# Optimization experiments

Measured on AMD Instinct MI355X. Metric: run time of the kernel, lower is better.

Reference implementation:

```python
import jax, jax.numpy as jnp
import numpy as np

N = 50000; E = 800000; T = 800000; G = 64
H = 128; IEMB = 128; BAS = 8; NS = 4; NR = 6; OEH = 128; OUT = 1; NB = 4; CUT = 5.0


def envelope(x):
    # exponent=5 -> p=6: 1/x + a*x^5 + b*x^6 + c*x^7 with a=-28, b=48, c=-21
    return 1.0 / x - 28.0 * x**5 + 48.0 * x**6 - 21.0 * x**7


def setup_inputs() -> dict:
    key = jax.random.key(0)
    ks = iter(jax.random.split(key, 80))
    def w(shape, s=0.1):
        return jax.random.normal(next(ks), shape, dtype=jnp.float32) * s
    inp = {}
    inp['z'] = jax.random.randint(next(ks), (N,), 0, 100, dtype=jnp.int32)
    inp['dist'] = jax.random.uniform(next(ks), (E,), jnp.float32, 0.05, 1.0)
    inp['dist_trip'] = jax.random.uniform(next(ks), (T,), jnp.float32, 0.05, 1.0)
    inp['angle'] = jax.random.uniform(next(ks), (T,), jnp.float32, -1.0, 1.0)
    inp['edge_index'] = jax.random.randint(next(ks), (2, E), 0, N, dtype=jnp.int32)
    inp['triplets'] = jax.random.randint(next(ks), (T, 3), 0, N, dtype=jnp.int32)
    inp['batch'] = jnp.sort(jax.random.randint(next(ks), (N,), 0, G, dtype=jnp.int32))
    inp['atom_table'] = w((100, H), 1.0)
    inp['rbf_freq'] = jnp.arange(1, NR + 1, dtype=jnp.float32) * jnp.float32(np.pi)
    inp['sbf_freq'] = jnp.arange(1, NR + 1, dtype=jnp.float32) * jnp.float32(np.pi)
    inp['emb_w1'] = w((NR, IEMB)); inp['emb_b1'] = w((IEMB,), 0.01)
    inp['emb_w2'] = w((IEMB, H)); inp['emb_b2'] = w((H,), 0.01)
    inp['iw_rbf1'] = w((NB, NR, BAS)); inp['iw_rbf2'] = w((NB, BAS, H))
    inp['iw_sbf1'] = w((NB, NS * NR, BAS)); inp['iw_sbf2'] = w((NB, BAS, IEMB))
    inp['iw_t1'] = w((NB, H, IEMB)); inp['iw_t2'] = w((NB, IEMB, H)); inp['ib_t2'] = w((NB, H), 0.01)
    inp['iw_up'] = w((NB, H, H)); inp['ib_up'] = w((NB, H), 0.01)
    inp['iw_down'] = w((NB, H, H)); inp['ib_down'] = w((NB, H), 0.01)
    inp['ow_rbf'] = w((NB + 1, NR, H))
    inp['ow0'] = w((NB + 1, H, OEH)); inp['ob0'] = w((NB + 1, OEH), 0.01)
    inp['ow1'] = w((NB + 1, OEH, OEH)); inp['ob1'] = w((NB + 1, OEH), 0.01)
    inp['ow2'] = w((NB + 1, OEH, OUT)); inp['ob2'] = w((NB + 1, OUT), 0.01)
    return inp


def _forward(atom_table, rbf_freq, sbf_freq, emb_w1, emb_b1, emb_w2, emb_b2,
             iw_rbf1, iw_rbf2, iw_sbf1, iw_sbf2, iw_t1, iw_t2, ib_t2,
             iw_up, ib_up, iw_down, ib_down, ow_rbf, ow0, ob0, ow1, ob1, ow2, ob2,
             dist, dist_trip, angle, z, edge_index, triplets, batch):
    row, col = edge_index[0], edge_index[1]
    j_idx = triplets[:, 1]
    # radial basis for edges: [E, NR]
    d = dist[:, None] / CUT
    rbf_e = envelope(d) * jnp.sin(rbf_freq * d)
    # spherical basis for triplets: [T, NS*NR]
    dt = dist_trip[:, None] / CUT
    rbf_t = envelope(dt) * jnp.sin(sbf_freq * dt)
    a = angle[:, None]
    sph = jnp.concatenate([jnp.ones_like(a), a, 0.5 * (3 * a**2 - 1), 0.5 * (5 * a**3 - 3 * a)], axis=-1)
    sbf_t = (rbf_t[:, None, :] * sph[:, :, None]).reshape(a.shape[0], -1)

    x = atom_table[z]  # [N, H]
    # EmbeddingBlock: edge msg from rbf only, scattered to col
    e = jax.nn.silu(rbf_e @ emb_w1 + emb_b1) @ emb_w2 + emb_b2
    x = x + jax.ops.segment_sum(e, col, num_segments=N)

    def out_block(k, x):
        rbf_emb = rbf_e @ ow_rbf[k]            # [E, H]
        h = jax.ops.segment_sum(x[row] * rbf_emb, col, num_segments=N)
        h = jax.nn.silu(h @ ow0[k] + ob0[k])
        h = jax.nn.silu(h @ ow1[k] + ob1[k])
        return h @ ow2[k] + ob2[k]             # [N, OUT]

    P = out_block(0, x)
    for b in range(NB):
        x_up = x @ iw_up[b] + ib_up[b]
        x_down = x @ iw_down[b] + ib_down[b]
        rbf_emb = jax.nn.silu(rbf_e @ iw_rbf1[b]) @ iw_rbf2[b]      # [E, H]
        x_edge = x_up[row] * rbf_emb                                  # [E, H]
        sbf_emb = jax.nn.silu(sbf_t @ iw_sbf1[b]) @ iw_sbf2[b]      # [T, H]
        t = jax.nn.silu(x_down @ iw_t1[b]) @ iw_t2[b] + ib_t2[b]     # [N, H]
        # original: for each triplet i, x_edge += t[j]*sbf_emb[i] (broadcast over all edges)
        extra = jnp.sum(t[j_idx] * sbf_emb, axis=0)                   # [H]
        x_edge = x_edge + extra
        x = x + jax.ops.segment_sum(x_edge, col, num_segments=N)
        P = P + out_block(b + 1, x)

    counts = jax.ops.segment_sum(jnp.ones((x.shape[0],), jnp.float32), batch, num_segments=G)
    pooled = jax.ops.segment_sum(P, batch, num_segments=G) / jnp.maximum(counts, 1.0)[:, None]
    return pooled  # [G, OUT]


def reference(z, dist, dist_trip, angle, edge_index, triplets, batch, atom_table, rbf_freq, sbf_freq,
              emb_w1, emb_b1, emb_w2, emb_b2, iw_rbf1, iw_rbf2, iw_sbf1, iw_sbf2, iw_t1, iw_t2, ib_t2,
              iw_up, ib_up, iw_down, ib_down, ow_rbf, ow0, ob0, ow1, ob1, ow2, ob2):
    return _forward(atom_table, rbf_freq, sbf_freq, emb_w1, emb_b1, emb_w2, emb_b2,
                    iw_rbf1, iw_rbf2, iw_sbf1, iw_sbf2, iw_t1, iw_t2, ib_t2,
                    iw_up, ib_up, iw_down, ib_down, ow_rbf, ow0, ob0, ow1, ob1, ow2, ob2,
                    dist, dist_trip, angle, z, edge_index, triplets, batch)
```

## Files before the change

kernel.cpp:

```cpp
#include <hip/hip_runtime.h>
#include <hip/hip_fp16.h>

#define N_ 50000
#define E_ 800000
#define T_ 800000
#define G_ 64
#define H_ 128

#define NBK 782
#define NSB (NBK * 8)
#define CAPS 512
#define CHUNK 4096
#define EB ((E_ + CHUNK - 1) / CHUNK)
#define TB ((T_ + CHUNK - 1) / CHUNK)
#define XSLOT 16

#define GEMMG2 ((N_ + 31) / 32)
#define NG2 ((N_ + 1) / 2)
#define NIX ((N_ * 16 + 127) / 128)
#define SVG ((N_ + 3) / 4)
#define EG ((E_ + 255) / 256)
#define TG ((T_ + 255) / 256)

typedef __attribute__((ext_vector_type(8))) short bf16x8;
typedef __attribute__((ext_vector_type(4))) float f32x4;
typedef _Float16 f16x2 __attribute__((ext_vector_type(2)));

__device__ __forceinline__ float siluf(float v) {
    return __fdividef(v, 1.0f + __expf(-v));
}

__device__ __forceinline__ unsigned short f2bf(float f) {
    unsigned int u = __float_as_uint(f);
    u += 0x7fffu + ((u >> 16) & 1u);
    return (unsigned short)(u >> 16);
}
__device__ __forceinline__ unsigned int f2bf2(float a, float b) {
    return (unsigned int)f2bf(a) | ((unsigned int)f2bf(b) << 16);
}
__device__ __forceinline__ float bf2f(unsigned short h) {
    return __uint_as_float(((unsigned int)h) << 16);
}
__device__ __forceinline__ float2 bf2x2(unsigned int p) {
    return make_float2(__uint_as_float(p << 16), __uint_as_float(p & 0xffff0000u));
}
__device__ __forceinline__ float fdot2f(f16x2 a, f16x2 b, float c) {
    return __builtin_amdgcn_fdot2(a, b, c, false);
}

__global__ __launch_bounds__(256) void k_bucket(const int* __restrict__ ecol,
                                                const int* __restrict__ trip,
                                                int* bcntE, unsigned int* __restrict__ ebkt,
                                                int* bcntT, unsigned int* __restrict__ tbkt) {
    __shared__ int hist[NBK];
    __shared__ int bbase[NBK];
    int blk = blockIdx.x;
    bool isE = blk < EB;
    int ebase = (isE ? blk : blk - EB) * CHUNK;
    const int nElem = isE ? E_ : T_;
    int r = blk & 7;
    int* bcnt = isE ? bcntE : bcntT;
    unsigned int* bkt = isE ? ebkt : tbkt;
    int tid = threadIdx.x;

    for (int i = tid; i < NBK; i += 256) hist[i] = 0;
    __syncthreads();

    int cols[16];
    #pragma unroll
    for (int u = 0; u < 16; ++u) {
        int idx = ebase + u * 256 + tid;
        int c = -1;
        if (idx < nElem) c = isE ? ecol[idx] : trip[3 * idx + 1];
        cols[u] = c;
        if (c >= 0) atomicAdd(&hist[c >> 6], 1);
    }
    __syncthreads();

    for (int b = tid; b < NBK; b += 256) {
        int c = hist[b];
        bbase[b] = c ? atomicAdd(&bcnt[b * 8 + r], c) : 0;
        hist[b] = 0;
    }
    __syncthreads();

    #pragma unroll
    for (int u = 0; u < 16; ++u) {
        int c = cols[u];
        if (c >= 0) {
            int bk = c >> 6;
            int off = atomicAdd(&hist[bk], 1);
            int pos = bbase[bk] + off;
            if (pos < CAPS) {
                int idx = ebase + u * 256 + tid;
                bkt[(size_t)(bk * 8 + r) * CAPS + pos] =
                    ((unsigned int)idx << 6) | (unsigned int)(c & 63);
            }
        }
    }
}

__global__ __launch_bounds__(1024) void k_scanB(const int* __restrict__ bcntE, int* bktbaseE,
                                                const int* __restrict__ bcntT, int* bktbaseT) {
    const int* bcnt = (blockIdx.x == 0) ? bcntE : bcntT;
    int* bb = (blockIdx.x == 0) ? bktbaseE : bktbaseT;
    int tid = threadIdx.x, lane = tid & 63, w = tid >> 6;
    __shared__ int wsum[16];
    int v = 0;
    if (tid < NBK) {
        #pragma unroll
        for (int s = 0; s < 8; ++s) v += min(bcnt[tid * 8 + s], CAPS);
    }
    int incl = v;
    #pragma unroll
    for (int s = 1; s < 64; s <<= 1) {
        int t = __shfl_up(incl, (unsigned)s, 64);
        if (lane >= s) incl += t;
    }
    if (lane == 63) wsum[w] = incl;
    __syncthreads();
    int wexcl = 0;
    for (int j = 0; j < w; ++j) wexcl += wsum[j];
    if (tid < NBK) bb[tid] = wexcl + incl - v;
}

__global__ __launch_bounds__(256) void k_place(const int* __restrict__ bcntE, const unsigned int* __restrict__ ebkt,
                                               const int* __restrict__ erow, const float* __restrict__ dist,
                                               const int* __restrict__ bktbaseE, int* __restrict__ rowptrE,
                                               int* __restrict__ slist, float* __restrict__ distS,
                                               const int* __restrict__ bcntT, const unsigned int* __restrict__ tbkt,
                                               const float* __restrict__ dist_trip, const float* __restrict__ angle,
                                               const int* __restrict__ bktbaseT, int* __restrict__ rowptrT,
                                               float2* __restrict__ tpay) {
    int b = blockIdx.x;
    bool isE = b < NBK;
    if (!isE) b -= NBK;
    int tid = threadIdx.x;
    __shared__ int ccnt[64];
    __shared__ int cbase[64];
    __shared__ int nb[8];
    if (tid < 64) ccnt[tid] = 0;
    const int* bcnt = isE ? bcntE : bcntT;
    const unsigned int* bkt = isE ? ebkt : tbkt;
    if (tid < 8) nb[tid] = min(bcnt[b * 8 + tid], CAPS);
    __syncthreads();
    for (int s = 0; s < 8; ++s) {
        int n = nb[s];
        const unsigned int* src = bkt + (size_t)(b * 8 + s) * CAPS;
        for (int i = tid; i < n; i += 256) atomicAdd(&ccnt[src[i] & 63u], 1);
    }
    __syncthreads();
    if (tid < 64) {
        int v = ccnt[tid];
        int incl = v;
        #pragma unroll
        for (int s = 1; s < 64; s <<= 1) {
            int t = __shfl_up(incl, (unsigned)s, 64);
            if (tid >= s) incl += t;
        }
        int base = (isE ? bktbaseE : bktbaseT)[b];
        int excl = base + incl - v;
        cbase[tid] = excl;
        int col = b * 64 + tid;
        int* rp = isE ? rowptrE : rowptrT;
        if (col <= N_) rp[col] = excl;
        ccnt[tid] = 0;
    }
    __syncthreads();
    for (int s = 0; s < 8; ++s) {
        int n = nb[s];
        const unsigned int* src = bkt + (size_t)(b * 8 + s) * CAPS;
        for (int i = tid; i < n; i += 256) {
            unsigned int rec = src[i];
            int c = (int)(rec & 63u);
            int e = (int)(rec >> 6);
            int off = atomicAdd(&ccnt[c], 1);
            int pos = cbase[c] + off;
            if (isE) {
                slist[pos] = erow[e];
                distS[pos] = dist[e];
            } else {
                tpay[pos] = make_float2(dist_trip[e], angle[e]);
            }
        }
    }
}

__global__ __launch_bounds__(256) void k_wprep(const float* __restrict__ emb_w2, const float* __restrict__ iw_down,
                                               const float* __restrict__ iw_t1, const float* __restrict__ iw_t2,
                                               const float* __restrict__ iw_up, const float* __restrict__ ow0,
                                               const float* __restrict__ ow1, unsigned short* __restrict__ Wt) {
    int mat = blockIdx.x >> 3;
    int part = blockIdx.x & 7;
    const float* src;
    if (mat == 0) src = emb_w2;
    else if (mat < 5) src = iw_down + (size_t)(mat - 1) * 16384;
    else if (mat < 9) src = iw_t1 + (size_t)(mat - 5) * 16384;
    else if (mat < 13) src = iw_t2 + (size_t)(mat - 9) * 16384;
    else if (mat < 17) src = iw_up + (size_t)(mat - 13) * 16384;
    else if (mat < 22) src = ow0 + (size_t)(mat - 17) * 16384;
    else src = ow1 + (size_t)(mat - 22) * 16384;
    unsigned short* dst = Wt + (size_t)mat * 16384;
    int base = part * 2048;
    for (int i = base + threadIdx.x; i < base + 2048; i += 256) {
        int k = i >> 7, n = i & 127;
        dst[n * 128 + k] = f2bf(src[i]);
    }
}

__global__ __launch_bounds__(256) void k_geomb(const float* __restrict__ distS,
                                               const float* __restrict__ freq, const float* __restrict__ iw_rbf1,
                                               float* __restrict__ rbfS, __half* __restrict__ s8all,
                                               const float2* __restrict__ tpay, const float* __restrict__ sfreq,
                                               __half* __restrict__ basis) {
    __shared__ float W1s[4][48];
    int tid = threadIdx.x;
    if (blockIdx.x < EG) {
        if (tid < 192) W1s[tid / 48][tid % 48] = iw_rbf1[tid];
        __syncthreads();
        int p = blockIdx.x * 256 + tid;
        if (p >= E_) return;
        float d = distS[p] * 0.2f;
        float d2 = d * d, d4 = d2 * d2, d5 = d4 * d;
        float env = __fdividef(1.0f, d) - 28.0f * d5 + 48.0f * d5 * d - 21.0f * d5 * d2;
        float rb[6];
        #pragma unroll
        for (int r = 0; r < 6; ++r) {
            rb[r] = env * __sinf(freq[r] * d);
            rbfS[(size_t)p * 6 + r] = rb[r];
        }
        #pragma unroll
        for (int b = 0; b < 4; ++b) {
            __half out[8];
            #pragma unroll
            for (int k = 0; k < 8; ++k) {
                float u = 0.f;
                #pragma unroll
                for (int r = 0; r < 6; ++r) u += rb[r] * W1s[b][r * 8 + k];
                out[k] = __float2half(siluf(u));
            }
            *(uint4*)&s8all[((size_t)b * E_ + p) * 8] = *(uint4*)out;
        }
    } else {
        int t = (blockIdx.x - EG) * 256 + tid;
        if (t >= T_) return;
        float2 da = tpay[t];
        float d = da.x * 0.2f;
        float a = da.y;
        float d2 = d * d, d4 = d2 * d2, d5 = d4 * d;
        float env = __fdividef(1.0f, d) - 28.0f * d5 + 48.0f * d5 * d - 21.0f * d5 * d2;
        float rb[6];
        #pragma unroll
        for (int r = 0; r < 6; ++r) rb[r] = env * __sinf(sfreq[r] * d);
        float sph[4];
        sph[0] = 1.0f; sph[1] = a; sph[2] = 1.5f * a * a - 0.5f; sph[3] = 2.5f * a * a * a - 1.5f * a;
        __half out[24];
        #pragma unroll
        for (int s = 0; s < 4; ++s)
            #pragma unroll
            for (int r = 0; r < 6; ++r) out[s * 6 + r] = __float2half(sph[s] * rb[r]);
        uint4* dst = (uint4*)(basis + (size_t)t * 24);
        dst[0] = ((uint4*)out)[0];
        dst[1] = ((uint4*)out)[1];
        dst[2] = ((uint4*)out)[2];
    }
}

__global__ __launch_bounds__(128) void k_embSix(const float* __restrict__ atab, const int* __restrict__ z,
                                                unsigned short* __restrict__ xh,
                                                const int* __restrict__ rowptr, const float* __restrict__ rbfS,
                                                const float* __restrict__ w1, const float* __restrict__ b1,
                                                unsigned short* __restrict__ SSh) {
    int tid = threadIdx.x;
    if (blockIdx.x < NIX) {
        int t = blockIdx.x * 128 + tid;
        if (t >= N_ * 16) return;
        int node = t >> 4, q = t & 15;
        const float4* a4 = (const float4*)atab;
        float4 v0 = a4[(size_t)z[node] * 32 + q * 2];
        float4 v1 = a4[(size_t)z[node] * 32 + q * 2 + 1];
        uint4 pk;
        pk.x = f2bf2(v0.x, v0.y);
        pk.y = f2bf2(v0.z, v0.w);
        pk.z = f2bf2(v1.x, v1.y);
        pk.w = f2bf2(v1.z, v1.w);
        ((uint4*)xh)[t] = pk;
    } else {
        int node = (blockIdx.x - NIX) * 2 + (tid >> 6);
        int lane = tid & 63;
        if (node >= N_) return;
        int c = lane * 2;
        float wc0[6], wc1[6];
        #pragma unroll
        for (int r = 0; r < 6; ++r) { wc0[r] = w1[r * 128 + c]; wc1[r] = w1[r * 128 + c + 1]; }
        float bb0 = b1[c], bb1 = b1[c + 1];
        float a0 = 0.f, a1 = 0.f;
        int p0 = rowptr[node], p1 = rowptr[node + 1];
        int p = p0;
        for (; p + 4 <= p1; p += 4) {
            float2 rb[4][3];
            #pragma unroll
            for (int u = 0; u < 4; ++u) {
                const float2* r2 = (const float2*)&rbfS[(size_t)(p + u) * 6];
                rb[u][0] = r2[0]; rb[u][1] = r2[1]; rb[u][2] = r2[2];
            }
            #pragma unroll
            for (int u = 0; u < 4; ++u) {
                float u0 = bb0 + rb[u][0].x * wc0[0] + rb[u][0].y * wc0[1] + rb[u][1].x * wc0[2] +
                           rb[u][1].y * wc0[3] + rb[u][2].x * wc0[4] + rb[u][2].y * wc0[5];
                float u1 = bb1 + rb[u][0].x * wc1[0] + rb[u][0].y * wc1[1] + rb[u][1].x * wc1[2] +
                           rb[u][1].y * wc1[3] + rb[u][2].x * wc1[4] + rb[u][2].y * wc1[5];
                a0 += siluf(u0);
                a1 += siluf(u1);
            }
        }
        for (; p < p1; ++p) {
            const float2* r2 = (const float2*)&rbfS[(size_t)p * 6];
            float2 ra = r2[0], rbx = r2[1], rc = r2[2];
            float u0 = bb0 + ra.x * wc0[0] + ra.y * wc0[1] + rbx.x * wc0[2] + rbx.y * wc0[3] + rc.x * wc0[4] + rc.y * wc0[5];
            float u1 = bb1 + ra.x * wc1[0] + ra.y * wc1[1] + rbx.x * wc1[2] + rbx.y * wc1[3] + rc.x * wc1[4] + rc.y * wc1[5];
            a0 += siluf(u0);
            a1 += siluf(u1);
        }
        *(unsigned int*)&SSh[(size_t)node * 128 + c] = f2bf2(a0, a1);
    }
}


__device__ __forceinline__ void body_gemm(int bid, const unsigned short* Ap, const unsigned short* Wt,
                                          const float* bias, const int* rp, unsigned short* Ch, int M) {
    int tid = threadIdx.x;
    int wave = tid >> 6, lane = tid & 63;
    int m15 = lane & 15, quad = lane >> 4;
    int row0 = bid * 32 + wave * 16;
    int arow = row0 + m15;
    if (arow > M - 1) arow = M - 1;

    f32x4 acc[8];
    #pragma unroll
    for (int nt = 0; nt < 8; ++nt) acc[nt] = (f32x4){0.f, 0.f, 0.f, 0.f};
    #pragma unroll
    for (int kt = 0; kt < 4; ++kt) {
        int ks = kt * 32 + quad * 8;
        bf16x8 av = *(const bf16x8*)(Ap + (size_t)arow * 128 + ks);
        #pragma unroll
        for (int nt = 0; nt < 8; ++nt) {
            bf16x8 bf = *(const bf16x8*)(Wt + (size_t)(nt * 16 + m15) * 128 + ks);
            acc[nt] = __builtin_amdgcn_mfma_f32_16x16x32_bf16(av, bf, acc[nt], 0, 0, 0);
        }
    }
    #pragma unroll
    for (int nt = 0; nt < 8; ++nt) {
        int col = nt * 16 + m15;
        float bc = bias[col];
        #pragma unroll
        for (int reg = 0; reg < 4; ++reg) {
            int row = row0 + quad * 4 + reg;
            if (row < M) {
                float v = acc[nt][reg] + bc * (float)(rp[row + 1] - rp[row]);
                v += bf2f(Ch[(size_t)row * 128 + col]);
                Ch[(size_t)row * 128 + col] = f2bf(v);
            }
        }
    }
}

__device__ __forceinline__ void body_sv4(int bid, const int* rowptrT, const __half* basis,
                                         const float* iw_sbf1, float* SV4, int n) {
    int tid = threadIdx.x;
    int wave = tid >> 6, lane = tid & 63;
    int node = bid * 4 + wave * 2 + (lane >> 5);
    int sub = lane & 31;
    int blk = sub >> 3, k = sub & 7;
    if (node >= n) return;
    const float* W1 = iw_sbf1 + blk * 192;
    f16x2 w[12];
    #pragma unroll
    for (int j = 0; j < 12; ++j) {
        f16x2 t;
        t.x = (_Float16)W1[(2 * j) * 8 + k];
        t.y = (_Float16)W1[(2 * j + 1) * 8 + k];
        w[j] = t;
    }
    float acc = 0.f;
    int p0 = rowptrT[node], p1 = rowptrT[node + 1];
    for (int p = p0; p < p1; ++p) {
        union { uint4 q[3]; f16x2 h[12]; } bs;
        const uint4* bp = (const uint4*)(basis + (size_t)p * 24);
        bs.q[0] = bp[0]; bs.q[1] = bp[1]; bs.q[2] = bp[2];
        float u = 0.f;
        #pragma unroll
        for (int j = 0; j < 12; ++j) u = fdot2f(bs.h[j], w[j], u);
        acc += siluf(u);
    }
    SV4[((size_t)blk * n + node) * 8 + k] = acc;
}

__device__ __forceinline__ void body_gather(int node0, const int* rowptr, const int* slist,
                                            const float* rbfS, const unsigned short* xh,
                                            const float* wrbf, unsigned short* hB, int n) {
    int tid = threadIdx.x;
    int node = node0 + (tid >> 6);
    int lane = tid & 63;
    if (node >= n) return;
    int c = lane * 2;
    float wc0[6], wc1[6];
    #pragma unroll
    for (int r = 0; r < 6; ++r) { wc0[r] = wrbf[r * 128 + c]; wc1[r] = wrbf[r * 128 + c + 1]; }
    float a0 = 0.f, a1 = 0.f;
    int p0 = rowptr[node], p1 = rowptr[node + 1];
    int p = p0;
    for (; p + 4 <= p1; p += 4) {
        int s0 = slist[p], s1 = slist[p + 1], s2 = slist[p + 2], s3 = slist[p + 3];
        float2 rb[4][3];
        #pragma unroll
        for (int u = 0; u < 4; ++u) {
            const float2* r2 = (const float2*)&rbfS[(size_t)(p + u) * 6];
            rb[u][0] = r2[0]; rb[u][1] = r2[1]; rb[u][2] = r2[2];
        }
        unsigned int xv0 = *(const unsigned int*)&xh[(size_t)s0 * 128 + c];
        unsigned int xv1 = *(const unsigned int*)&xh[(size_t)s1 * 128 + c];
        unsigned int xv2 = *(const unsigned int*)&xh[(size_t)s2 * 128 + c];
        unsigned int xv3 = *(const unsigned int*)&xh[(size_t)s3 * 128 + c];
        #pragma unroll
        for (int u = 0; u < 4; ++u) {
            float e0 = rb[u][0].x * wc0[0] + rb[u][0].y * wc0[1] + rb[u][1].x * wc0[2] +
                       rb[u][1].y * wc0[3] + rb[u][2].x * wc0[4] + rb[u][2].y * wc0[5];
            float e1 = rb[u][0].x * wc1[0] + rb[u][0].y * wc1[1] + rb[u][1].x * wc1[2] +
                       rb[u][1].y * wc1[3] + rb[u][2].x * wc1[4] + rb[u][2].y * wc1[5];
            float2 xf = bf2x2((u == 0) ? xv0 : (u == 1) ? xv1 : (u == 2) ? xv2 : xv3);
            a0 += xf.x * e0;
            a1 += xf.y * e1;
        }
    }
    for (; p < p1; ++p) {
        int src = slist[p];
        const float2* r2 = (const float2*)&rbfS[(size_t)p * 6];
        float2 ra = r2[0], rbx = r2[1], rc = r2[2];
        float e0 = ra.x * wc0[0] + ra.y * wc0[1] + rbx.x * wc0[2] + rbx.y * wc0[3] + rc.x * wc0[4] + rc.y * wc0[5];
        float e1 = ra.x * wc1[0] + ra.y * wc1[1] + rbx.x * wc1[2] + rbx.y * wc1[3] + rc.x * wc1[4] + rc.y * wc1[5];
        float2 xf = bf2x2(*(const unsigned int*)&xh[(size_t)src * 128 + c]);
        a0 += xf.x * e0;
        a1 += xf.y * e1;
    }
    *(unsigned int*)&hB[(size_t)node * 128 + c] = f2bf2(a0, a1);
}

__device__ __forceinline__ void body_block_mlp(int bid, unsigned short* smh,
                                               const unsigned short* xh,
                                               const unsigned short* Wd, const float* bd,
                                               const unsigned short* Wt1,
                                               const unsigned short* Wt2, const float* bt2,
                                               const unsigned short* Wup, const float* bup,
                                               const float* SV, const float* W2,
                                               float* extraP, unsigned short* xuph, int M) {
    int tid = threadIdx.x;
    int wave = tid >> 6, lane = tid & 63;
    int m15 = lane & 15, quad = lane >> 4;
    int row0 = bid * 32 + wave * 16;
    int arow = row0 + m15;
    if (arow > M - 1) arow = M - 1;
    unsigned short* L = smh + wave * (16 * 136);

    f32x4 accD[8], accU[8];
    #pragma unroll
    for (int nt = 0; nt < 8; ++nt) { accD[nt] = (f32x4){0.f, 0.f, 0.f, 0.f}; accU[nt] = (f32x4){0.f, 0.f, 0.f, 0.f}; }
    #pragma unroll
    for (int kt = 0; kt < 4; ++kt) {
        int ks = kt * 32 + quad * 8;
        bf16x8 av = *(const bf16x8*)(xh + (size_t)arow * 128 + ks);
        #pragma unroll
        for (int nt = 0; nt < 8; ++nt) {
            bf16x8 bd_ = *(const bf16x8*)(Wd + (size_t)(nt * 16 + m15) * 128 + ks);
            accD[nt] = __builtin_amdgcn_mfma_f32_16x16x32_bf16(av, bd_, accD[nt], 0, 0, 0);
            bf16x8 bu_ = *(const bf16x8*)(Wup + (size_t)(nt * 16 + m15) * 128 + ks);
            accU[nt] = __builtin_amdgcn_mfma_f32_16x16x32_bf16(av, bu_, accU[nt], 0, 0, 0);
        }
    }
    #pragma unroll
    for (int nt = 0; nt < 8; ++nt) {
        int col = nt * 16 + m15;
        float bcu = bup[col], bcd = bd[col];
        #pragma unroll
        for (int reg = 0; reg < 4; ++reg) {
            int row = row0 + quad * 4 + reg;
            if (row < M) xuph[(size_t)row * 128 + col] = f2bf(accU[nt][reg] + bcu);
            L[(quad * 4 + reg) * 136 + col] = f2bf(accD[nt][reg] + bcd);
        }
    }
    __syncthreads();

    #pragma unroll
    for (int nt = 0; nt < 8; ++nt) accD[nt] = (f32x4){0.f, 0.f, 0.f, 0.f};
    #pragma unroll
    for (int kt = 0; kt < 4; ++kt) {
        int ks = kt * 32 + quad * 8;
        bf16x8 av = *(const bf16x8*)(L + m15 * 136 + ks);
        #pragma unroll
        for (int nt = 0; nt < 8; ++nt) {
            bf16x8 bf = *(const bf16x8*)(Wt1 + (size_t)(nt * 16 + m15) * 128 + ks);
            accD[nt] = __builtin_amdgcn_mfma_f32_16x16x32_bf16(av, bf, accD[nt], 0, 0, 0);
        }
    }
    __syncthreads();
    #pragma unroll
    for (int nt = 0; nt < 8; ++nt) {
        int col = nt * 16 + m15;
        #pragma unroll
        for (int reg = 0; reg < 4; ++reg)
            L[(quad * 4 + reg) * 136 + col] = f2bf(siluf(accD[nt][reg]));
    }
    __syncthreads();

    #pragma unroll
    for (int nt = 0; nt < 8; ++nt) accD[nt] = (f32x4){0.f, 0.f, 0.f, 0.f};
    #pragma unroll
    for (int kt = 0; kt < 4; ++kt) {
        int ks = kt * 32 + quad * 8;
        bf16x8 av = *(const bf16x8*)(L + m15 * 136 + ks);
        #pragma unroll
        for (int nt = 0; nt < 8; ++nt) {
            bf16x8 bf = *(const bf16x8*)(Wt2 + (size_t)(nt * 16 + m15) * 128 + ks);
            accD[nt] = __builtin_amdgcn_mfma_f32_16x16x32_bf16(av, bf, accD[nt], 0, 0, 0);
        }
    }
    __syncthreads();
    #pragma unroll
    for (int nt = 0; nt < 8; ++nt) {
        int col = nt * 16 + m15;
        float bc = bt2[col];
        #pragma unroll
        for (int reg = 0; reg < 4; ++reg)
            smh[(wave * 16 + quad * 4 + reg) * 136 + col] = f2bf(accD[nt][reg] + bc);
    }
    __syncthreads();

    int col = tid;
    float acc8[8];
    #pragma unroll
    for (int k = 0; k < 8; ++k) acc8[k] = 0.f;
    int rmax = M - bid * 32;
    if (rmax > 32) rmax = 32;
    for (int rr = 0; rr < rmax; ++rr) {
        float t = bf2f(smh[rr * 136 + col]);
        const float4* sv4 = (const float4*)&SV[(size_t)(bid * 32 + rr) * 8];
        float4 s0 = sv4[0], s1 = sv4[1];
        acc8[0] += t * s0.x; acc8[1] += t * s0.y; acc8[2] += t * s0.z; acc8[3] += t * s0.w;
        acc8[4] += t * s1.x; acc8[5] += t * s1.y; acc8[6] += t * s1.z; acc8[7] += t * s1.w;
    }
    float e = 0.f;
    #pragma unroll
    for (int k = 0; k < 8; ++k) e += acc8[k] * W2[k * 128 + col];
    atomicAdd(&extraP[(bid & (XSLOT - 1)) * 128 + col], e);
}

template <int PACC>
__device__ __forceinline__ void body_out_mlp(int bid, unsigned short* smh,
                                             const unsigned short* hB,
                                             const unsigned short* W0t, const float* b0,
                                             const unsigned short* W1t, const float* b1,
                                             const float* w2col, const float* ob2p,
                                             float* Pout, int M) {
    int tid = threadIdx.x;
    int wave = tid >> 6, lane = tid & 63;
    int m15 = lane & 15, quad = lane >> 4;
    int row0 = bid * 32 + wave * 16;
    int arow = row0 + m15;
    if (arow > M - 1) arow = M - 1;
    unsigned short* L = smh + wave * (16 * 136);

    f32x4 acc[8];
    #pragma unroll
    for (int nt = 0; nt < 8; ++nt) acc[nt] = (f32x4){0.f, 0.f, 0.f, 0.f};
    #pragma unroll
    for (int kt = 0; kt < 4; ++kt) {
        int ks = kt * 32 + quad * 8;
        bf16x8 av = *(const bf16x8*)(hB + (size_t)arow * 128 + ks);
        #pragma unroll
        for (int nt = 0; nt < 8; ++nt) {
            bf16x8 bf = *(const bf16x8*)(W0t + (size_t)(nt * 16 + m15) * 128 + ks);
            acc[nt] = __builtin_amdgcn_mfma_f32_16x16x32_bf16(av, bf, acc[nt], 0, 0, 0);
        }
    }
    #pragma unroll
    for (int nt = 0; nt < 8; ++nt) {
        int col = nt * 16 + m15;
        float bc = b0[col];
        #pragma unroll
        for (int reg = 0; reg < 4; ++reg)
            L[(quad * 4 + reg) * 136 + col] = f2bf(siluf(acc[nt][reg] + bc));
    }
    __syncthreads();

    #pragma unroll
    for (int nt = 0; nt < 8; ++nt) acc[nt] = (f32x4){0.f, 0.f, 0.f, 0.f};
    #pragma unroll
    for (int kt = 0; kt < 4; ++kt) {
        int ks = kt * 32 + quad * 8;
        bf16x8 av = *(const bf16x8*)(L + m15 * 136 + ks);
        #pragma unroll
        for (int nt = 0; nt < 8; ++nt) {
            bf16x8 bf = *(const bf16x8*)(W1t + (size_t)(nt * 16 + m15) * 128 + ks);
            acc[nt] = __builtin_amdgcn_mfma_f32_16x16x32_bf16(av, bf, acc[nt], 0, 0, 0);
        }
    }
    float w2c[8], pp[4];
    #pragma unroll
    for (int nt = 0; nt < 8; ++nt) w2c[nt] = w2col[nt * 16 + m15];
    #pragma unroll
    for (int reg = 0; reg < 4; ++reg) pp[reg] = 0.f;
    #pragma unroll
    for (int nt = 0; nt < 8; ++nt) {
        float bc = b1[nt * 16 + m15];
        #pragma unroll
        for (int reg = 0; reg < 4; ++reg)
            pp[reg] += siluf(acc[nt][reg] + bc) * w2c[nt];
    }
    #pragma unroll
    for (int reg = 0; reg < 4; ++reg) {
        float s = pp[reg];
        s += __shfl_xor(s, 1, 64);
        s += __shfl_xor(s, 2, 64);
        s += __shfl_xor(s, 4, 64);
        s += __shfl_xor(s, 8, 64);
        if (m15 == 0) {
            int row = row0 + quad * 4 + reg;
            if (row < M) {
                float r = s + ob2p[0];
                if (PACC == 2) r += Pout[row];
                Pout[row] = r;
            }
        }
    }
}

__device__ __forceinline__ void body_interact(int node0, float* exs,
                                              const int* rowptr, const int* slist,
                                              const __half* s8, const float* W2,
                                              const float* extraP,
                                              const unsigned short* xuph,
                                              unsigned short* xh, int n) {
    int tid = threadIdx.x;
    {
        float s = 0.f;
        #pragma unroll
        for (int q = 0; q < XSLOT; ++q) s += extraP[q * 128 + tid];
        exs[tid] = s;
    }
    __syncthreads();
    int node = node0 + (tid >> 6);
    int lane = tid & 63;
    if (node >= n) return;
    int c = lane * 2;
    f16x2 w2a[4], w2b[4];
    #pragma unroll
    for (int j = 0; j < 4; ++j) {
        f16x2 wa, wb;
        wa.x = (_Float16)W2[(2 * j) * 128 + c];
        wa.y = (_Float16)W2[(2 * j + 1) * 128 + c];
        wb.x = (_Float16)W2[(2 * j) * 128 + c + 1];
        wb.y = (_Float16)W2[(2 * j + 1) * 128 + c + 1];
        w2a[j] = wa;
        w2b[j] = wb;
    }
    int p0 = rowptr[node], p1 = rowptr[node + 1];
    float cntf = (float)(p1 - p0);
    float a0 = cntf * exs[c], a1 = cntf * exs[c + 1];
    int p = p0;
    for (; p + 4 <= p1; p += 4) {
        int s0 = slist[p], s1 = slist[p + 1], s2 = slist[p + 2], s3 = slist[p + 3];
        uint4 sv[4];
        #pragma unroll
        for (int u = 0; u < 4; ++u) sv[u] = *(const uint4*)(s8 + (size_t)(p + u) * 8);
        unsigned int xv0 = *(const unsigned int*)&xuph[(size_t)s0 * 128 + c];
        unsigned int xv1 = *(const unsigned int*)&xuph[(size_t)s1 * 128 + c];
        unsigned int xv2 = *(const unsigned int*)&xuph[(size_t)s2 * 128 + c];
        unsigned int xv3 = *(const unsigned int*)&xuph[(size_t)s3 * 128 + c];
        #pragma unroll
        for (int u = 0; u < 4; ++u) {
            union { uint4 q; f16x2 h[4]; } s;
            s.q = sv[u];
            float e0 = fdot2f(s.h[0], w2a[0], 0.f);
            e0 = fdot2f(s.h[1], w2a[1], e0);
            e0 = fdot2f(s.h[2], w2a[2], e0);
            e0 = fdot2f(s.h[3], w2a[3], e0);
            float e1 = fdot2f(s.h[0], w2b[0], 0.f);
            e1 = fdot2f(s.h[1], w2b[1], e1);
            e1 = fdot2f(s.h[2], w2b[2], e1);
            e1 = fdot2f(s.h[3], w2b[3], e1);
            float2 xf = bf2x2((u == 0) ? xv0 : (u == 1) ? xv1 : (u == 2) ? xv2 : xv3);
            a0 += xf.x * e0;
            a1 += xf.y * e1;
        }
    }
    for (; p < p1; ++p) {
        int src = slist[p];
        float2 xf = bf2x2(*(const unsigned int*)&xuph[(size_t)src * 128 + c]);
        union { uint4 q; f16x2 h[4]; } s;
        s.q = *(const uint4*)(s8 + (size_t)p * 8);
        float e0 = fdot2f(s.h[0], w2a[0], 0.f);
        e0 = fdot2f(s.h[1], w2a[1], e0);
        e0 = fdot2f(s.h[2], w2a[2], e0);
        e0 = fdot2f(s.h[3], w2a[3], e0);
        float e1 = fdot2f(s.h[0], w2b[0], 0.f);
        e1 = fdot2f(s.h[1], w2b[1], e1);
        e1 = fdot2f(s.h[2], w2b[2], e1);
        e1 = fdot2f(s.h[3], w2b[3], e1);
        a0 += xf.x * e0;
        a1 += xf.y * e1;
    }
    unsigned int cur = *(unsigned int*)&xh[(size_t)node * 128 + c];
    float2 xc = bf2x2(cur);
    *(unsigned int*)&xh[(size_t)node * 128 + c] = f2bf2(xc.x + a0, xc.y + a1);
}


__global__ __launch_bounds__(128) void k_gemmsv(const unsigned short* __restrict__ Ap,
                                                const unsigned short* __restrict__ Wt,
                                                const float* __restrict__ bias, const int* __restrict__ rp,
                                                unsigned short* __restrict__ Ch,
                                                const int* __restrict__ rowptrT, const __half* __restrict__ basis,
                                                const float* __restrict__ iw_sbf1, float* __restrict__ SV4) {
    if (blockIdx.x < GEMMG2)
        body_gemm(blockIdx.x, Ap, Wt, bias, rp, Ch, N_);
    else
        body_sv4(blockIdx.x - GEMMG2, rowptrT, basis, iw_sbf1, SV4, N_);
}

__global__ __launch_bounds__(128) void k_fuse_gb(const unsigned short* __restrict__ xh,
                                                 const unsigned short* __restrict__ Wd, const float* __restrict__ bd,
                                                 const unsigned short* __restrict__ Wt1,
                                                 const unsigned short* __restrict__ Wt2, const float* __restrict__ bt2,
                                                 const unsigned short* __restrict__ Wup, const float* __restrict__ bup,
                                                 const float* __restrict__ SV, const float* __restrict__ W2,
                                                 float* __restrict__ extraP, unsigned short* __restrict__ xuph,
                                                 const int* __restrict__ rowptr, const int* __restrict__ slist,
                                                 const float* __restrict__ rbfS, const float* __restrict__ wrbf,
                                                 unsigned short* __restrict__ hB) {
    __shared__ unsigned short smh[2 * 16 * 136];
    if (blockIdx.x < GEMMG2)
        body_block_mlp(blockIdx.x, smh, xh, Wd, bd, Wt1, Wt2, bt2, Wup, bup, SV, W2, extraP, xuph, N_);
    else
        body_gather((blockIdx.x - GEMMG2) * 2, rowptr, slist, rbfS, xh, wrbf, hB, N_);
}

template <int PACC>
__global__ __launch_bounds__(128) void k_fuse_mi(const unsigned short* __restrict__ hB,
                                                 const unsigned short* __restrict__ W0t, const float* __restrict__ b0,
                                                 const unsigned short* __restrict__ W1t, const float* __restrict__ b1,
                                                 const float* __restrict__ w2col, const float* __restrict__ ob2p,
                                                 float* __restrict__ Pout,
                                                 const int* __restrict__ rowptr, const int* __restrict__ slist,
                                                 const __half* __restrict__ s8, const float* __restrict__ W2,
                                                 const float* __restrict__ extraP,
                                                 const unsigned short* __restrict__ xuph,
                                                 unsigned short* __restrict__ xh) {
    __shared__ unsigned short smh[2 * 16 * 136];
    if (blockIdx.x < GEMMG2)
        body_out_mlp<PACC>(blockIdx.x, smh, hB, W0t, b0, W1t, b1, w2col, ob2p, Pout, N_);
    else
        body_interact((blockIdx.x - GEMMG2) * 2, (float*)smh, rowptr, slist, s8, W2, extraP, xuph, xh, N_);
}

__global__ __launch_bounds__(128) void k_gather1(const int* __restrict__ rowptr, const int* __restrict__ slist,
                                                 const float* __restrict__ rbfS, const unsigned short* __restrict__ xh,
                                                 const float* __restrict__ wrbf, unsigned short* __restrict__ hB) {
    body_gather(blockIdx.x * 2, rowptr, slist, rbfS, xh, wrbf, hB, N_);
}
__global__ __launch_bounds__(128) void k_mlp1(const unsigned short* __restrict__ hB,
                                              const unsigned short* __restrict__ W0t, const float* __restrict__ b0,
                                              const unsigned short* __restrict__ W1t, const float* __restrict__ b1,
                                              const float* __restrict__ w2col, const float* __restrict__ ob2p,
                                              float* __restrict__ Pout) {
    __shared__ unsigned short smh[2 * 16 * 136];
    body_out_mlp<2>(blockIdx.x, smh, hB, W0t, b0, W1t, b1, w2col, ob2p, Pout, N_);
}

__global__ __launch_bounds__(256) void k_pool(const float* __restrict__ P, const int* __restrict__ batch,
                                              float* __restrict__ pool, float* __restrict__ cnt, int n) {
    int i = blockIdx.x * 256 + threadIdx.x;
    int lane = threadIdx.x & 63;
    int b = (i < n) ? batch[i] : -1;
    float p = (i < n) ? P[i] : 0.f;
    int b0 = __shfl(b, 0, 64);
    int b63 = __shfl(b, 63, 64);
    if (b0 == b63 && b0 >= 0) {
        float s = p;
        #pragma unroll
        for (int off = 32; off > 0; off >>= 1) s += __shfl_xor(s, off, 64);
        if (lane == 0) {
            atomicAdd(&pool[b0], s);
            atomicAdd(&cnt[b0], 64.0f);
        }
    } else {
        if (i < n) {
            atomicAdd(&pool[b], p);
            atomicAdd(&cnt[b], 1.0f);
        }
    }
}

__global__ __launch_bounds__(64) void k_final(const float* __restrict__ pool, const float* __restrict__ cnt,
                                              float* __restrict__ out) {
    int g = threadIdx.x;
    if (g < G_) out[g] = __fdividef(pool[g], fmaxf(cnt[g], 1.0f));
}

extern "C" void kernel_launch(void* const* d_in, const int* in_sizes, int n_in,
                              void* d_out, int out_size, void* d_ws, size_t ws_size,
                              hipStream_t stream) {
    (void)in_sizes; (void)n_in; (void)out_size; (void)ws_size;
    const int* z = (const int*)d_in[0];
    const float* dist = (const float*)d_in[1];
    const float* dist_trip = (const float*)d_in[2];
    const float* angle = (const float*)d_in[3];
    const int* edge_index = (const int*)d_in[4];
    const int* triplets = (const int*)d_in[5];
    const int* batch = (const int*)d_in[6];
    const float* atom_table = (const float*)d_in[7];
    const float* rbf_freq = (const float*)d_in[8];
    const float* sbf_freq = (const float*)d_in[9];
    const float* emb_w1 = (const float*)d_in[10];
    const float* emb_b1 = (const float*)d_in[11];
    const float* emb_w2 = (const float*)d_in[12];
    const float* emb_b2 = (const float*)d_in[13];
    const float* iw_rbf1 = (const float*)d_in[14];
    const float* iw_rbf2 = (const float*)d_in[15];
    const float* iw_sbf1 = (const float*)d_in[16];
    const float* iw_sbf2 = (const float*)d_in[17];
    const float* iw_t1 = (const float*)d_in[18];
    const float* iw_t2 = (const float*)d_in[19];
    const float* ib_t2 = (const float*)d_in[20];
    const float* iw_up = (const float*)d_in[21];
    const float* ib_up = (const float*)d_in[22];
    const float* iw_down = (const float*)d_in[23];
    const float* ib_down = (const float*)d_in[24];
    const float* ow_rbf = (const float*)d_in[25];
    const float* ow0 = (const float*)d_in[26];
    const float* ob0 = (const float*)d_in[27];
    const float* ow1 = (const float*)d_in[28];
    const float* ob1 = (const float*)d_in[29];
    const float* ow2 = (const float*)d_in[30];
    const float* ob2 = (const float*)d_in[31];

    const int* erow = edge_index;
    const int* ecol = edge_index + E_;

    float* ws = (float*)d_ws;
    float* bufA = ws;
    float* bufB = bufA + (size_t)N_ * H_;
    float* P = bufB + (size_t)N_ * H_;
    float* rbfS = P + N_;
    float* SV4 = rbfS + (size_t)E_ * 6;
    float* extra4 = SV4 + (size_t)4 * N_ * 8;
    float* pool = extra4 + 4 * XSLOT * 128;
    float* cnt = pool + G_;
    int* bcntE = (int*)(cnt + G_);
    int* bcntT = bcntE + NSB;
    int* bktbaseE = bcntT + NSB;
    int* bktbaseT = bktbaseE + NBK;
    int* rowptr = bktbaseT + NBK;
    int* rowptrT = rowptr + N_ + 1;
    int* slist = rowptrT + N_ + 1;
    float* distS = (float*)(slist + E_);
    uintptr_t tp = (uintptr_t)(distS + E_);
    tp = (tp + 7) & ~(uintptr_t)7;
    float2* tpay = (float2*)tp;
    __half* s8all = (__half*)(tpay + T_);
    __half* basis = s8all + (size_t)4 * E_ * 8;
    unsigned short* xh = (unsigned short*)(basis + (size_t)T_ * 24);
    unsigned short* xuph = xh + (size_t)N_ * H_;
    unsigned short* Wt = xuph + (size_t)N_ * H_;
    unsigned short* hB = (unsigned short*)bufB;

    unsigned int* ebkt = (unsigned int*)s8all;
    unsigned int* tbkt = ebkt + (size_t)NSB * CAPS;

    hipMemsetAsync(extra4, 0, (4 * XSLOT * 128 + 2 * G_ + 2 * NSB) * sizeof(float), stream);
    k_wprep<<<27 * 8, 256, 0, stream>>>(emb_w2, iw_down, iw_t1, iw_t2, iw_up, ow0, ow1, Wt);
    k_bucket<<<EB + TB, 256, 0, stream>>>(ecol, triplets, bcntE, ebkt, bcntT, tbkt);
    k_scanB<<<2, 1024, 0, stream>>>(bcntE, bktbaseE, bcntT, bktbaseT);
    k_place<<<2 * NBK, 256, 0, stream>>>(bcntE, ebkt, erow, dist, bktbaseE, rowptr, slist, distS,
                                         bcntT, tbkt, dist_trip, angle, bktbaseT, rowptrT, tpay);

    k_geomb<<<EG + TG, 256, 0, stream>>>(distS, rbf_freq, iw_rbf1, rbfS, s8all,
                                         tpay, sbf_freq, basis);
    k_embSix<<<NIX + NG2, 128, 0, stream>>>(atom_table, z, xh, rowptr, rbfS, emb_w1, emb_b1,
                                            (unsigned short*)bufA);
    k_gemmsv<<<GEMMG2 + SVG, 128, 0, stream>>>((unsigned short*)bufA, Wt, emb_b2, rowptr, xh,
                                               rowptrT, basis, iw_sbf1, SV4);

    for (int b = 0; b < 4; ++b) {
        k_fuse_gb<<<GEMMG2 + NG2, 128, 0, stream>>>(xh,
                                                    Wt + (size_t)(1 + b) * 16384, ib_down + b * 128,
                                                    Wt + (size_t)(5 + b) * 16384,
                                                    Wt + (size_t)(9 + b) * 16384, ib_t2 + b * 128,
                                                    Wt + (size_t)(13 + b) * 16384, ib_up + b * 128,
                                                    SV4 + (size_t)b * N_ * 8,
                                                    iw_sbf2 + (size_t)b * 1024,
                                                    extra4 + (size_t)b * XSLOT * 128,
                                                    xuph,
                                                    rowptr, slist, rbfS,
                                                    ow_rbf + (size_t)b * 6 * 128, hB);
        if (b == 0)
            k_fuse_mi<1><<<GEMMG2 + NG2, 128, 0, stream>>>(hB,
                                                           Wt + (size_t)(17 + b) * 16384, ob0 + b * 128,
                                                           Wt + (size_t)(22 + b) * 16384, ob1 + b * 128,
                                                           ow2 + b * 128, ob2 + b, P,
                                                           rowptr, slist, s8all + (size_t)b * E_ * 8,
                                                           iw_rbf2 + (size_t)b * 1024,
                                                           extra4 + (size_t)b * XSLOT * 128,
                                                           xuph, xh);
        else
            k_fuse_mi<2><<<GEMMG2 + NG2, 128, 0, stream>>>(hB,
                                                           Wt + (size_t)(17 + b) * 16384, ob0 + b * 128,
                                                           Wt + (size_t)(22 + b) * 16384, ob1 + b * 128,
                                                           ow2 + b * 128, ob2 + b, P,
                                                           rowptr, slist, s8all + (size_t)b * E_ * 8,
                                                           iw_rbf2 + (size_t)b * 1024,
                                                           extra4 + (size_t)b * XSLOT * 128,
                                                           xuph, xh);
    }

    k_gather1<<<NG2, 128, 0, stream>>>(rowptr, slist, rbfS, xh, ow_rbf + (size_t)4 * 6 * 128, hB);
    k_mlp1<<<GEMMG2, 128, 0, stream>>>(hB, Wt + (size_t)21 * 16384, ob0 + 4 * 128,
                                       Wt + (size_t)26 * 16384, ob1 + 4 * 128,
                                       ow2 + 4 * 128, ob2 + 4, P);

    k_pool<<<(N_ + 255) / 256, 256, 0, stream>>>(P, batch, pool, cnt, N_);
    k_final<<<1, 64, 0, stream>>>(pool, cnt, (float*)d_out);
}
```

Before: 1.533 ms.

## Regroup per-block kernels: separate gathers, fuse block MLP with output MLP

Each interaction block used to launch two heterogeneous kernels: one ran the block MLP alongside the output gather, the other ran the output MLP alongside the interaction. They are now split by kind into three launches per block: a standalone output gather, a fused block-MLP-plus-output-MLP GEMM kernel, and a standalone interaction kernel, with the gather and interact kernels using 256-thread blocks covering 4 nodes each. The aim is to put homogeneous work in each launch and to chain the two dense MLPs through shared memory in one kernel. The cost is one more launch per block and less overlap between the memory-bound gather work and the MFMA-bound GEMM work.

```diff
diff --git a/kernel.cpp b/kernel.cpp
--- a/kernel.cpp
+++ b/kernel.cpp
@@ -17,6 +17,7 @@
 
 #define GEMMG2 ((N_ + 31) / 32)
 #define NG2 ((N_ + 1) / 2)
+#define NG4 ((N_ + 3) / 4)
 #define NIX ((N_ * 16 + 127) / 128)
 #define SVG ((N_ + 3) / 4)
 #define EG ((E_ + 255) / 256)
@@ -326,7 +327,6 @@
     }
 }
 
-
 __device__ __forceinline__ void body_gemm(int bid, const unsigned short* Ap, const unsigned short* Wt,
                                           const float* bias, const int* rp, unsigned short* Ch, int M) {
     int tid = threadIdx.x;
@@ -396,54 +396,16 @@
     SV4[((size_t)blk * n + node) * 8 + k] = acc;
 }
 
-__device__ __forceinline__ void body_gather(int node0, const int* rowptr, const int* slist,
-                                            const float* rbfS, const unsigned short* xh,
-                                            const float* wrbf, unsigned short* hB, int n) {
-    int tid = threadIdx.x;
-    int node = node0 + (tid >> 6);
-    int lane = tid & 63;
-    if (node >= n) return;
-    int c = lane * 2;
-    float wc0[6], wc1[6];
-    #pragma unroll
-    for (int r = 0; r < 6; ++r) { wc0[r] = wrbf[r * 128 + c]; wc1[r] = wrbf[r * 128 + c + 1]; }
-    float a0 = 0.f, a1 = 0.f;
-    int p0 = rowptr[node], p1 = rowptr[node + 1];
-    int p = p0;
-    for (; p + 4 <= p1; p += 4) {
-        int s0 = slist[p], s1 = slist[p + 1], s2 = slist[p + 2], s3 = slist[p + 3];
-        float2 rb[4][3];
-        #pragma unroll
-        for (int u = 0; u < 4; ++u) {
-            const float2* r2 = (const float2*)&rbfS[(size_t)(p + u) * 6];
-            rb[u][0] = r2[0]; rb[u][1] = r2[1]; rb[u][2] = r2[2];
-        }
-        unsigned int xv0 = *(const unsigned int*)&xh[(size_t)s0 * 128 + c];
-        unsigned int xv1 = *(const unsigned int*)&xh[(size_t)s1 * 128 + c];
-        unsigned int xv2 = *(const unsigned int*)&xh[(size_t)s2 * 128 + c];
-        unsigned int xv3 = *(const unsigned int*)&xh[(size_t)s3 * 128 + c];
-        #pragma unroll
-        for (int u = 0; u < 4; ++u) {
-            float e0 = rb[u][0].x * wc0[0] + rb[u][0].y * wc0[1] + rb[u][1].x * wc0[2] +
-                       rb[u][1].y * wc0[3] + rb[u][2].x * wc0[4] + rb[u][2].y * wc0[5];
-            float e1 = rb[u][0].x * wc1[0] + rb[u][0].y * wc1[1] + rb[u][1].x * wc1[2] +
-                       rb[u][1].y * wc1[3] + rb[u][2].x * wc1[4] + rb[u][2].y * wc1[5];
-            float2 xf = bf2x2((u == 0) ? xv0 : (u == 1) ? xv1 : (u == 2) ? xv2 : xv3);
-            a0 += xf.x * e0;
-            a1 += xf.y * e1;
-        }
-    }
-    for (; p < p1; ++p) {
-        int src = slist[p];
-        const float2* r2 = (const float2*)&rbfS[(size_t)p * 6];
-        float2 ra = r2[0], rbx = r2[1], rc = r2[2];
-        float e0 = ra.x * wc0[0] + ra.y * wc0[1] + rbx.x * wc0[2] + rbx.y * wc0[3] + rc.x * wc0[4] + rc.y * wc0[5];
-        float e1 = ra.x * wc1[0] + ra.y * wc1[1] + rbx.x * wc1[2] + rbx.y * wc1[3] + rc.x * wc1[4] + rc.y * wc1[5];
-        float2 xf = bf2x2(*(const unsigned int*)&xh[(size_t)src * 128 + c]);
-        a0 += xf.x * e0;
-        a1 += xf.y * e1;
-    }
-    *(unsigned int*)&hB[(size_t)node * 128 + c] = f2bf2(a0, a1);
+__global__ __launch_bounds__(128) void k_gemmsv(const unsigned short* __restrict__ Ap,
+                                                const unsigned short* __restrict__ Wt,
+                                                const float* __restrict__ bias, const int* __restrict__ rp,
+                                                unsigned short* __restrict__ Ch,
+                                                const int* __restrict__ rowptrT, const __half* __restrict__ basis,
+                                                const float* __restrict__ iw_sbf1, float* __restrict__ SV4) {
+    if (blockIdx.x < GEMMG2)
+        body_gemm(blockIdx.x, Ap, Wt, bias, rp, Ch, N_);
+    else
+        body_sv4(blockIdx.x - GEMMG2, rowptrT, basis, iw_sbf1, SV4, N_);
 }
 
 __device__ __forceinline__ void body_block_mlp(int bid, unsigned short* smh,
@@ -634,21 +596,100 @@
     }
 }
 
-__device__ __forceinline__ void body_interact(int node0, float* exs,
-                                              const int* rowptr, const int* slist,
-                                              const __half* s8, const float* W2,
-                                              const float* extraP,
-                                              const unsigned short* xuph,
-                                              unsigned short* xh, int n) {
+template <int PACC>
+__global__ __launch_bounds__(128) void k_mlp2(const unsigned short* __restrict__ xh,
+                                              const unsigned short* __restrict__ Wd, const float* __restrict__ bd,
+                                              const unsigned short* __restrict__ Wt1,
+                                              const unsigned short* __restrict__ Wt2, const float* __restrict__ bt2,
+                                              const unsigned short* __restrict__ Wup, const float* __restrict__ bup,
+                                              const float* __restrict__ SV, const float* __restrict__ W2,
+                                              float* __restrict__ extraP, unsigned short* __restrict__ xuph,
+                                              const unsigned short* __restrict__ hB,
+                                              const unsigned short* __restrict__ W0t, const float* __restrict__ b0,
+                                              const unsigned short* __restrict__ W1t, const float* __restrict__ b1,
+                                              const float* __restrict__ w2col, const float* __restrict__ ob2p,
+                                              float* __restrict__ Pout) {
+    __shared__ unsigned short smh[2 * 16 * 136];
+    body_block_mlp(blockIdx.x, smh, xh, Wd, bd, Wt1, Wt2, bt2, Wup, bup, SV, W2, extraP, xuph, N_);
+    __syncthreads();
+    body_out_mlp<PACC>(blockIdx.x, smh, hB, W0t, b0, W1t, b1, w2col, ob2p, Pout, N_);
+}
+
+__global__ __launch_bounds__(128) void k_out_mlp1(const unsigned short* __restrict__ hB,
+                                                  const unsigned short* __restrict__ W0t, const float* __restrict__ b0,
+                                                  const unsigned short* __restrict__ W1t, const float* __restrict__ b1,
+                                                  const float* __restrict__ w2col, const float* __restrict__ ob2p,
+                                                  float* __restrict__ Pout) {
+    __shared__ unsigned short smh[2 * 16 * 136];
+    body_out_mlp<2>(blockIdx.x, smh, hB, W0t, b0, W1t, b1, w2col, ob2p, Pout, N_);
+}
+
+__global__ __launch_bounds__(256) void k_out_gather(const int* __restrict__ rowptr, const int* __restrict__ slist,
+                                                    const float* __restrict__ rbfS,
+                                                    const unsigned short* __restrict__ xh,
+                                                    const float* __restrict__ wrbf,
+                                                    unsigned short* __restrict__ hB, int n) {
+    int node = blockIdx.x * 4 + (threadIdx.x >> 6);
+    int lane = threadIdx.x & 63;
+    if (node >= n) return;
+    int c = lane * 2;
+    float wc0[6], wc1[6];
+    #pragma unroll
+    for (int r = 0; r < 6; ++r) { wc0[r] = wrbf[r * 128 + c]; wc1[r] = wrbf[r * 128 + c + 1]; }
+    float a0 = 0.f, a1 = 0.f;
+    int p0 = rowptr[node], p1 = rowptr[node + 1];
+    int p = p0;
+    for (; p + 4 <= p1; p += 4) {
+        int s0 = slist[p], s1 = slist[p + 1], s2 = slist[p + 2], s3 = slist[p + 3];
+        float2 rb[4][3];
+        #pragma unroll
+        for (int u = 0; u < 4; ++u) {
+            const float2* r2 = (const float2*)&rbfS[(size_t)(p + u) * 6];
+            rb[u][0] = r2[0]; rb[u][1] = r2[1]; rb[u][2] = r2[2];
+        }
+        unsigned int xv0 = *(const unsigned int*)&xh[(size_t)s0 * 128 + c];
+        unsigned int xv1 = *(const unsigned int*)&xh[(size_t)s1 * 128 + c];
+        unsigned int xv2 = *(const unsigned int*)&xh[(size_t)s2 * 128 + c];
+        unsigned int xv3 = *(const unsigned int*)&xh[(size_t)s3 * 128 + c];
+        #pragma unroll
+        for (int u = 0; u < 4; ++u) {
+            float e0 = rb[u][0].x * wc0[0] + rb[u][0].y * wc0[1] + rb[u][1].x * wc0[2] +
+                       rb[u][1].y * wc0[3] + rb[u][2].x * wc0[4] + rb[u][2].y * wc0[5];
+            float e1 = rb[u][0].x * wc1[0] + rb[u][0].y * wc1[1] + rb[u][1].x * wc1[2] +
+                       rb[u][1].y * wc1[3] + rb[u][2].x * wc1[4] + rb[u][2].y * wc1[5];
+            float2 xf = bf2x2((u == 0) ? xv0 : (u == 1) ? xv1 : (u == 2) ? xv2 : xv3);
+            a0 += xf.x * e0;
+            a1 += xf.y * e1;
+        }
+    }
+    for (; p < p1; ++p) {
+        int src = slist[p];
+        const float2* r2 = (const float2*)&rbfS[(size_t)p * 6];
+        float2 ra = r2[0], rbx = r2[1], rc = r2[2];
+        float e0 = ra.x * wc0[0] + ra.y * wc0[1] + rbx.x * wc0[2] + rbx.y * wc0[3] + rc.x * wc0[4] + rc.y * wc0[5];
+        float e1 = ra.x * wc1[0] + ra.y * wc1[1] + rbx.x * wc1[2] + rbx.y * wc1[3] + rc.x * wc1[4] + rc.y * wc1[5];
+        float2 xf = bf2x2(*(const unsigned int*)&xh[(size_t)src * 128 + c]);
+        a0 += xf.x * e0;
+        a1 += xf.y * e1;
+    }
+    *(unsigned int*)&hB[(size_t)node * 128 + c] = f2bf2(a0, a1);
+}
+
+__global__ __launch_bounds__(256) void k_interact(const int* __restrict__ rowptr, const int* __restrict__ slist,
+                                                  const __half* __restrict__ s8, const float* __restrict__ W2,
+                                                  const float* __restrict__ extraP,
+                                                  const unsigned short* __restrict__ xuph,
+                                                  unsigned short* __restrict__ xh, int n) {
+    __shared__ float exs[128];
     int tid = threadIdx.x;
-    {
+    if (tid < 128) {
         float s = 0.f;
         #pragma unroll
         for (int q = 0; q < XSLOT; ++q) s += extraP[q * 128 + tid];
         exs[tid] = s;
     }
     __syncthreads();
-    int node = node0 + (tid >> 6);
+    int node = blockIdx.x * 4 + (tid >> 6);
     int lane = tid & 63;
     if (node >= n) return;
     int c = lane * 2;
@@ -712,68 +753,6 @@
     unsigned int cur = *(unsigned int*)&xh[(size_t)node * 128 + c];
     float2 xc = bf2x2(cur);
     *(unsigned int*)&xh[(size_t)node * 128 + c] = f2bf2(xc.x + a0, xc.y + a1);
-}
-
-
-__global__ __launch_bounds__(128) void k_gemmsv(const unsigned short* __restrict__ Ap,
-                                                const unsigned short* __restrict__ Wt,
-                                                const float* __restrict__ bias, const int* __restrict__ rp,
-                                                unsigned short* __restrict__ Ch,
-                                                const int* __restrict__ rowptrT, const __half* __restrict__ basis,
-                                                const float* __restrict__ iw_sbf1, float* __restrict__ SV4) {
-    if (blockIdx.x < GEMMG2)
-        body_gemm(blockIdx.x, Ap, Wt, bias, rp, Ch, N_);
-    else
-        body_sv4(blockIdx.x - GEMMG2, rowptrT, basis, iw_sbf1, SV4, N_);
-}
-
-__global__ __launch_bounds__(128) void k_fuse_gb(const unsigned short* __restrict__ xh,
-                                                 const unsigned short* __restrict__ Wd, const float* __restrict__ bd,
-                                                 const unsigned short* __restrict__ Wt1,
-                                                 const unsigned short* __restrict__ Wt2, const float* __restrict__ bt2,
-                                                 const unsigned short* __restrict__ Wup, const float* __restrict__ bup,
-                                                 const float* __restrict__ SV, const float* __restrict__ W2,
-                                                 float* __restrict__ extraP, unsigned short* __restrict__ xuph,
-                                                 const int* __restrict__ rowptr, const int* __restrict__ slist,
-                                                 const float* __restrict__ rbfS, const float* __restrict__ wrbf,
-                                                 unsigned short* __restrict__ hB) {
-    __shared__ unsigned short smh[2 * 16 * 136];
-    if (blockIdx.x < GEMMG2)
-        body_block_mlp(blockIdx.x, smh, xh, Wd, bd, Wt1, Wt2, bt2, Wup, bup, SV, W2, extraP, xuph, N_);
-    else
-        body_gather((blockIdx.x - GEMMG2) * 2, rowptr, slist, rbfS, xh, wrbf, hB, N_);
-}
-
-template <int PACC>
-__global__ __launch_bounds__(128) void k_fuse_mi(const unsigned short* __restrict__ hB,
-                                                 const unsigned short* __restrict__ W0t, const float* __restrict__ b0,
-                                                 const unsigned short* __restrict__ W1t, const float* __restrict__ b1,
-                                                 const float* __restrict__ w2col, const float* __restrict__ ob2p,
-                                                 float* __restrict__ Pout,
-                                                 const int* __restrict__ rowptr, const int* __restrict__ slist,
-                                                 const __half* __restrict__ s8, const float* __restrict__ W2,
-                                                 const float* __restrict__ extraP,
-                                                 const unsigned short* __restrict__ xuph,
-                                                 unsigned short* __restrict__ xh) {
-    __shared__ unsigned short smh[2 * 16 * 136];
-    if (blockIdx.x < GEMMG2)
-        body_out_mlp<PACC>(blockIdx.x, smh, hB, W0t, b0, W1t, b1, w2col, ob2p, Pout, N_);
-    else
-        body_interact((blockIdx.x - GEMMG2) * 2, (float*)smh, rowptr, slist, s8, W2, extraP, xuph, xh, N_);
-}
-
-__global__ __launch_bounds__(128) void k_gather1(const int* __restrict__ rowptr, const int* __restrict__ slist,
-                                                 const float* __restrict__ rbfS, const unsigned short* __restrict__ xh,
-                                                 const float* __restrict__ wrbf, unsigned short* __restrict__ hB) {
-    body_gather(blockIdx.x * 2, rowptr, slist, rbfS, xh, wrbf, hB, N_);
-}
-__global__ __launch_bounds__(128) void k_mlp1(const unsigned short* __restrict__ hB,
-                                              const unsigned short* __restrict__ W0t, const float* __restrict__ b0,
-                                              const unsigned short* __restrict__ W1t, const float* __restrict__ b1,
-                                              const float* __restrict__ w2col, const float* __restrict__ ob2p,
-                                              float* __restrict__ Pout) {
-    __shared__ unsigned short smh[2 * 16 * 136];
-    body_out_mlp<2>(blockIdx.x, smh, hB, W0t, b0, W1t, b1, w2col, ob2p, Pout, N_);
 }
 
 __global__ __launch_bounds__(256) void k_pool(const float* __restrict__ P, const int* __restrict__ batch,
@@ -891,41 +870,42 @@
                                                rowptrT, basis, iw_sbf1, SV4);
 
     for (int b = 0; b < 4; ++b) {
-        k_fuse_gb<<<GEMMG2 + NG2, 128, 0, stream>>>(xh,
-                                                    Wt + (size_t)(1 + b) * 16384, ib_down + b * 128,
-                                                    Wt + (size_t)(5 + b) * 16384,
-                                                    Wt + (size_t)(9 + b) * 16384, ib_t2 + b * 128,
-                                                    Wt + (size_t)(13 + b) * 16384, ib_up + b * 128,
-                                                    SV4 + (size_t)b * N_ * 8,
-                                                    iw_sbf2 + (size_t)b * 1024,
-                                                    extra4 + (size_t)b * XSLOT * 128,
-                                                    xuph,
-                                                    rowptr, slist, rbfS,
-                                                    ow_rbf + (size_t)b * 6 * 128, hB);
+        k_out_gather<<<NG4, 256, 0, stream>>>(rowptr, slist, rbfS, xh,
+                                              ow_rbf + (size_t)b * 6 * 128, hB, N_);
         if (b == 0)
-            k_fuse_mi<1><<<GEMMG2 + NG2, 128, 0, stream>>>(hB,
-                                                           Wt + (size_t)(17 + b) * 16384, ob0 + b * 128,
-                                                           Wt + (size_t)(22 + b) * 16384, ob1 + b * 128,
-                                                           ow2 + b * 128, ob2 + b, P,
-                                                           rowptr, slist, s8all + (size_t)b * E_ * 8,
-                                                           iw_rbf2 + (size_t)b * 1024,
-                                                           extra4 + (size_t)b * XSLOT * 128,
-                                                           xuph, xh);
+            k_mlp2<1><<<GEMMG2, 128, 0, stream>>>(xh,
+                                                  Wt + (size_t)(1 + b) * 16384, ib_down + b * 128,
+                                                  Wt + (size_t)(5 + b) * 16384,
+                                                  Wt + (size_t)(9 + b) * 16384, ib_t2 + b * 128,
+                                                  Wt + (size_t)(13 + b) * 16384, ib_up + b * 128,
+                                                  SV4 + (size_t)b * N_ * 8,
+                                                  iw_sbf2 + (size_t)b * 1024,
+                                                  extra4 + (size_t)b * XSLOT * 128, xuph,
+                                                  hB, Wt + (size_t)(17 + b) * 16384, ob0 + b * 128,
+                                                  Wt + (size_t)(22 + b) * 16384, ob1 + b * 128,
+                                                  ow2 + b * 128, ob2 + b, P);
         else
-            k_fuse_mi<2><<<GEMMG2 + NG2, 128, 0, stream>>>(hB,
-                                                           Wt + (size_t)(17 + b) * 16384, ob0 + b * 128,
-                                                           Wt + (size_t)(22 + b) * 16384, ob1 + b * 128,
-                                                           ow2 + b * 128, ob2 + b, P,
-                                                           rowptr, slist, s8all + (size_t)b * E_ * 8,
-                                                           iw_rbf2 + (size_t)b * 1024,
-                                                           extra4 + (size_t)b * XSLOT * 128,
-                                                           xuph, xh);
-    }
-
-    k_gather1<<<NG2, 128, 0, stream>>>(rowptr, slist, rbfS, xh, ow_rbf + (size_t)4 * 6 * 128, hB);
-    k_mlp1<<<GEMMG2, 128, 0, stream>>>(hB, Wt + (size_t)21 * 16384, ob0 + 4 * 128,
-                                       Wt + (size_t)26 * 16384, ob1 + 4 * 128,
-                                       ow2 + 4 * 128, ob2 + 4, P);
+            k_mlp2<2><<<GEMMG2, 128, 0, stream>>>(xh,
+                                                  Wt + (size_t)(1 + b) * 16384, ib_down + b * 128,
+                                                  Wt + (size_t)(5 + b) * 16384,
+                                                  Wt + (size_t)(9 + b) * 16384, ib_t2 + b * 128,
+                                                  Wt + (size_t)(13 + b) * 16384, ib_up + b * 128,
+                                                  SV4 + (size_t)b * N_ * 8,
+                                                  iw_sbf2 + (size_t)b * 1024,
+                                                  extra4 + (size_t)b * XSLOT * 128, xuph,
+                                                  hB, Wt + (size_t)(17 + b) * 16384, ob0 + b * 128,
+                                                  Wt + (size_t)(22 + b) * 16384, ob1 + b * 128,
+                                                  ow2 + b * 128, ob2 + b, P);
+        k_interact<<<NG4, 256, 0, stream>>>(rowptr, slist, s8all + (size_t)b * E_ * 8,
+                                            iw_rbf2 + (size_t)b * 1024, extra4 + (size_t)b * XSLOT * 128,
+                                            xuph, xh, N_);
+    }
+
+    k_out_gather<<<NG4, 256, 0, stream>>>(rowptr, slist, rbfS, xh,
+                                          ow_rbf + (size_t)4 * 6 * 128, hB, N_);
+    k_out_mlp1<<<GEMMG2, 128, 0, stream>>>(hB, Wt + (size_t)21 * 16384, ob0 + 4 * 128,
+                                           Wt + (size_t)26 * 16384, ob1 + 4 * 128,
+                                           ow2 + 4 * 128, ob2 + 4, P);
 
     k_pool<<<(N_ + 255) / 256, 256, 0, stream>>>(P, batch, pool, cnt, N_);
     k_final<<<1, 64, 0, stream>>>(pool, cnt, (float*)d_out);
```

Measured after the change: 1.419 ms (median of 2 runs). 7.4% less time.
